# Kernel optimization log

Hardware: AMD Instinct MI355X
Metric: run time of the kernel (lower is better)

Reference implementation:

```python
import jax, jax.numpy as jnp
import numpy as np

GROUPS = 8


def setup_inputs() -> dict:
    key = jax.random.key(0)
    k1, k2, k3 = jax.random.split(key, 3)
    B, H, W, Cin, Cout, KH, KW = 32, 56, 56, 256, 256, 3, 3
    inputs = jax.random.normal(k1, (B, H, W, Cin), dtype=jnp.float32)
    # HWIO kernel for grouped conv: input channel dim = Cin // groups
    fan_in = KH * KW * (Cin // GROUPS)
    limit = np.sqrt(6.0 / (fan_in + Cout // GROUPS))  # glorot-ish scale
    kernel = jax.random.uniform(k2, (KH, KW, Cin // GROUPS, Cout), dtype=jnp.float32,
                                minval=-limit, maxval=limit)
    bias = jnp.zeros((Cout,), dtype=jnp.float32)
    return {"inputs": inputs, "kernel": kernel, "bias": bias}


def reference(inputs, kernel, bias):
    # Equivalent to per-group slice + Conv2D + concat: a single grouped conv.
    # inputs: [B,H,W,Cin] NHWC; kernel: [KH,KW,Cin//G,Cout] HWIO
    out = jax.lax.conv_general_dilated(
        inputs, kernel,
        window_strides=(1, 1),
        padding="SAME",
        lhs_dilation=(1, 1),
        rhs_dilation=(1, 1),
        dimension_numbers=("NHWC", "HWIO", "NHWC"),
        feature_group_count=GROUPS,
    )
    out = out + bias  # broadcast over [B,H,W,Cout]
    return out
```

## Files before the change

kernel.cpp:

```cpp
#include <hip/hip_runtime.h>


#define R_ 8
#define TPW 7

typedef __bf16 bf16x8 __attribute__((ext_vector_type(8)));
typedef float floatx4 __attribute__((ext_vector_type(4)));
typedef unsigned short ushortx4 __attribute__((ext_vector_type(4)));

__device__ __forceinline__ unsigned short f2bf(float f) {
    unsigned int u = __builtin_bit_cast(unsigned int, f);
    u += 0x7fffu + ((u >> 16) & 1u);
    return (unsigned short)(u >> 16);
}

__global__ __launch_bounds__(256)
void wprep(const float* __restrict__ wgt, unsigned short* __restrict__ wbf) {
    const int i = blockIdx.x * 256 + threadIdx.x;
    const int co256 = i & 255;
    const int tmp   = i >> 8;
    const int ci    = tmp & 31;
    const int kk    = tmp >> 5;
    const int g  = co256 >> 5;
    const int co = co256 & 31;
    wbf[((g * 9 + kk) * 32 + co) * 32 + ci] = f2bf(wgt[i]);
}

__global__ __launch_bounds__(256, 4)
void gconv_mfma(const float* __restrict__ in, const unsigned short* __restrict__ wbf,
                const float* __restrict__ bias, float* __restrict__ out) {
    const int rt = blockIdx.x;
    const int g  = blockIdx.y;
    const int b  = blockIdx.z;
    const int y0 = rt * R_;

    __shared__ unsigned short lds_in[10 * 58 * 32];

    const int tid = threadIdx.x;

    float4 v[19];
#pragma unroll
    for (int i = 0; i < 19; ++i) {
        const int c   = tid + (i << 8);
        const int row = c / 464;
        const int rem = c - row * 464;
        const int gy  = y0 - 1 + row;
        const int gx  = (rem >> 3) - 1;
        const bool ok = (c < 4640) & ((unsigned)gy < 56u) & ((unsigned)gx < 56u);
        const int gidx = ok ? ((((b * 56 + gy) * 56 + gx) << 8) + (g << 5) + ((rem & 7) << 2))
                            : 0;
        v[i] = *reinterpret_cast<const float4*>(&in[gidx]);
    }
#pragma unroll
    for (int i = 0; i < 19; ++i) {
        const int c = tid + (i << 8);
        if (c < 4640) {
            const int row = c / 464;
            const int rem = c - row * 464;
            const int gy  = y0 - 1 + row;
            const int gx  = (rem >> 3) - 1;
            float4 w = v[i];
            if (!(((unsigned)gy < 56u) & ((unsigned)gx < 56u)))
                w = make_float4(0.f, 0.f, 0.f, 0.f);
            ushortx4 p;
            p.x = f2bf(w.x); p.y = f2bf(w.y); p.z = f2bf(w.z); p.w = f2bf(w.w);
            *reinterpret_cast<ushortx4*>(
                &lds_in[(row * 58 + (rem >> 3)) * 32 + ((rem & 7) << 2)]) = p;
        }
    }

    __syncthreads();

    const int wv   = tid >> 6;
    const int lane = tid & 63;
    const int lc   = lane & 15;
    const int quad = lane >> 4;

    int lane_base[TPW];
#pragma unroll
    for (int t = 0; t < TPW; ++t) {
        const int p  = (wv * TPW + t) * 16 + lc;
        const int yl = p / 56;
        const int xl = p - yl * 56;
        lane_base[t] = (yl * 58 + xl) * 32 + (quad << 3);
    }

    const unsigned short* wq = &wbf[(g * 9 * 32) * 32 + (quad << 3)];

    floatx4 acc[TPW][2];
#pragma unroll
    for (int t = 0; t < TPW; ++t) {
        acc[t][0] = (floatx4)(0.f);
        acc[t][1] = (floatx4)(0.f);
    }

    bf16x8 b0 = *reinterpret_cast<const bf16x8*>(&wq[(0 * 32 + lc) * 32]);
    bf16x8 b1 = *reinterpret_cast<const bf16x8*>(&wq[(0 * 32 + 16 + lc) * 32]);

#pragma unroll
    for (int kk = 0; kk < 9; ++kk) {
        const int ky = kk / 3, kx = kk % 3;
        const int koff = (ky * 58 + kx) * 32;
        bf16x8 nb0 = b0, nb1 = b1;
        if (kk < 8) {
            nb0 = *reinterpret_cast<const bf16x8*>(&wq[((kk + 1) * 32 + lc) * 32]);
            nb1 = *reinterpret_cast<const bf16x8*>(&wq[((kk + 1) * 32 + 16 + lc) * 32]);
        }
#pragma unroll
        for (int t = 0; t < TPW; ++t) {
            const bf16x8 a = *reinterpret_cast<const bf16x8*>(&lds_in[lane_base[t] + koff]);
            acc[t][0] = __builtin_amdgcn_mfma_f32_16x16x32_bf16(b0, a, acc[t][0], 0, 0, 0);
            acc[t][1] = __builtin_amdgcn_mfma_f32_16x16x32_bf16(b1, a, acc[t][1], 0, 0, 0);
        }
        b0 = nb0; b1 = nb1;
    }

    const float4 bv0 = *reinterpret_cast<const float4*>(&bias[(g << 5) + (quad << 2)]);
    const float4 bv1 = *reinterpret_cast<const float4*>(&bias[(g << 5) + 16 + (quad << 2)]);
    const int obase = (((b * 56 + y0) * 56) << 8) + (g << 5) + (quad << 2);
#pragma unroll
    for (int t = 0; t < TPW; ++t) {
        const int p = (wv * TPW + t) * 16 + lc;
        const int y = p / 56;
        const int x = p - y * 56;
        float* o = &out[obase + ((y * 56 + x) << 8)];
        float4 s0, s1;
        s0.x = acc[t][0][0] + bv0.x; s0.y = acc[t][0][1] + bv0.y;
        s0.z = acc[t][0][2] + bv0.z; s0.w = acc[t][0][3] + bv0.w;
        s1.x = acc[t][1][0] + bv1.x; s1.y = acc[t][1][1] + bv1.y;
        s1.z = acc[t][1][2] + bv1.z; s1.w = acc[t][1][3] + bv1.w;
        *reinterpret_cast<float4*>(o)      = s0;
        *reinterpret_cast<float4*>(o + 16) = s1;
    }
}

__global__ __launch_bounds__(256, 2)
void gconv_mfma_ldsw(const float* __restrict__ in, const float* __restrict__ wgt,
                     const float* __restrict__ bias, float* __restrict__ out) {
    const int rt = blockIdx.x, g = blockIdx.y, b = blockIdx.z;
    const int y0 = rt * R_;
    __shared__ unsigned short lds_in[10 * 58 * 32];
    __shared__ unsigned short lds_w[9 * 32 * 32];
    const int tid = threadIdx.x;
    for (int i = tid; i < 9 * 32 * 32; i += 256) {
        const int co = i & 31, ci = (i >> 5) & 31, kk = i >> 10;
        lds_w[(kk * 32 + co) * 32 + ci] = f2bf(wgt[(kk * 32 + ci) * 256 + g * 32 + co]);
    }
    for (int c = tid; c < 10 * 58 * 8; c += 256) {
        const int row = c / 464, rem = c - row * 464, col = rem >> 3, q = rem & 7;
        const int gy = y0 - 1 + row, gx = col - 1;
        float4 v = make_float4(0.f, 0.f, 0.f, 0.f);
        if ((unsigned)gy < 56u && (unsigned)gx < 56u)
            v = *reinterpret_cast<const float4*>(&in[(((b * 56 + gy) * 56 + gx) * 256) + g * 32 + q * 4]);
        ushortx4 p;
        p.x = f2bf(v.x); p.y = f2bf(v.y); p.z = f2bf(v.z); p.w = f2bf(v.w);
        *reinterpret_cast<ushortx4*>(&lds_in[(row * 58 + col) * 32 + q * 4]) = p;
    }
    __syncthreads();
    const int wv = tid >> 6, lane = tid & 63, lc = lane & 15, quad = lane >> 4;
    int lane_base[TPW];
#pragma unroll
    for (int t = 0; t < TPW; ++t) {
        const int p = (wv * TPW + t) * 16 + lc;
        const int yl = p / 56, xl = p - yl * 56;
        lane_base[t] = (yl * 58 + xl) * 32 + quad * 8;
    }
    floatx4 acc[TPW][2];
#pragma unroll
    for (int t = 0; t < TPW; ++t) { acc[t][0] = (floatx4)(0.f); acc[t][1] = (floatx4)(0.f); }
#pragma unroll
    for (int kk = 0; kk < 9; ++kk) {
        const int ky = kk / 3, kx = kk % 3;
        const int koff = (ky * 58 + kx) * 32;
        const bf16x8 bf0 = *reinterpret_cast<const bf16x8*>(&lds_w[(kk * 32 + lc) * 32 + quad * 8]);
        const bf16x8 bf1 = *reinterpret_cast<const bf16x8*>(&lds_w[(kk * 32 + 16 + lc) * 32 + quad * 8]);
#pragma unroll
        for (int t = 0; t < TPW; ++t) {
            const bf16x8 a = *reinterpret_cast<const bf16x8*>(&lds_in[lane_base[t] + koff]);
            acc[t][0] = __builtin_amdgcn_mfma_f32_16x16x32_bf16(a, bf0, acc[t][0], 0, 0, 0);
            acc[t][1] = __builtin_amdgcn_mfma_f32_16x16x32_bf16(a, bf1, acc[t][1], 0, 0, 0);
        }
    }
    const float bv0 = bias[g * 32 + lc], bv1 = bias[g * 32 + 16 + lc];
#pragma unroll
    for (int t = 0; t < TPW; ++t)
#pragma unroll
        for (int r = 0; r < 4; ++r) {
            const int p = (wv * TPW + t) * 16 + quad * 4 + r;
            const int y = p / 56, x = p - y * 56;
            float* o = &out[(((b * 56) + y0 + y) * 56 + x) * 256 + g * 32];
            o[lc] = acc[t][0][r] + bv0;
            o[16 + lc] = acc[t][1][r] + bv1;
        }
}

extern "C" void kernel_launch(void* const* d_in, const int* in_sizes, int n_in,
                              void* d_out, int out_size, void* d_ws, size_t ws_size,
                              hipStream_t stream) {
    const float* in   = (const float*)d_in[0];
    const float* wgt  = (const float*)d_in[1];
    const float* bias = (const float*)d_in[2];
    float* out        = (float*)d_out;
    dim3 grid(7, 8, 32);

    if (ws_size >= (size_t)(8 * 9 * 32 * 32 * sizeof(unsigned short))) {
        unsigned short* wbf = (unsigned short*)d_ws;
        wprep<<<dim3(288, 1, 1), dim3(256, 1, 1), 0, stream>>>(wgt, wbf);
        gconv_mfma<<<grid, dim3(256, 1, 1), 0, stream>>>(in, wbf, bias, out);
    } else {
        gconv_mfma_ldsw<<<grid, dim3(256, 1, 1), 0, stream>>>(in, wgt, bias, out);
    }
}
```

Measured before the change: 197.7 us.

## Make conv blocks persistent over row tiles with double-buffered LDS prefetch

Replaces the one-tile-per-block grouped conv with a kernel of 512 blocks. Each block handles one (batch, group) pair and walks 3 or 4 row tiles, alternating by parity. While the MFMAs run on the current tile, it loads the next tile's input from global memory into registers, then writes it into a second LDS buffer. Weights for all 9 taps are held in registers once per block, which removes the repeated weight loads. In exchange, LDS use doubles, occupancy drops to 2 blocks per unit, and the 3-versus-4 tile split leaves the work unevenly balanced.

```diff
diff --git a/kernel.cpp b/kernel.cpp
--- a/kernel.cpp
+++ b/kernel.cpp
@@ -3,6 +3,7 @@
 
 #define R_ 8
 #define TPW 7
+#define NLOAD 19
 
 typedef __bf16 bf16x8 __attribute__((ext_vector_type(8)));
 typedef float floatx4 __attribute__((ext_vector_type(4)));
@@ -26,111 +27,126 @@
     wbf[((g * 9 + kk) * 32 + co) * 32 + ci] = f2bf(wgt[i]);
 }
 
-__global__ __launch_bounds__(256, 4)
-void gconv_mfma(const float* __restrict__ in, const unsigned short* __restrict__ wbf,
+__global__ __launch_bounds__(256, 2)
+void gconv_pipe(const float* __restrict__ in, const unsigned short* __restrict__ wbf,
                 const float* __restrict__ bias, float* __restrict__ out) {
-    const int rt = blockIdx.x;
-    const int g  = blockIdx.y;
-    const int b  = blockIdx.z;
-    const int y0 = rt * R_;
-
-    __shared__ unsigned short lds_in[10 * 58 * 32];
-
-    const int tid = threadIdx.x;
-
-    float4 v[19];
-#pragma unroll
-    for (int i = 0; i < 19; ++i) {
-        const int c   = tid + (i << 8);
-        const int row = c / 464;
-        const int rem = c - row * 464;
-        const int gy  = y0 - 1 + row;
-        const int gx  = (rem >> 3) - 1;
-        const bool ok = (c < 4640) & ((unsigned)gy < 56u) & ((unsigned)gx < 56u);
-        const int gidx = ok ? ((((b * 56 + gy) * 56 + gx) << 8) + (g << 5) + ((rem & 7) << 2))
-                            : 0;
-        v[i] = *reinterpret_cast<const float4*>(&in[gidx]);
-    }
-#pragma unroll
-    for (int i = 0; i < 19; ++i) {
-        const int c = tid + (i << 8);
-        if (c < 4640) {
+    const int h  = blockIdx.x & 1;
+    const int gb = blockIdx.x >> 1;
+    const int g  = gb & 7;
+    const int b  = gb >> 3;
+    const int ntiles = 4 - h;
+
+    __shared__ unsigned short lds_in[2][10 * 58 * 32];
+
+    const int tid  = threadIdx.x;
+    const int lane = tid & 63;
+    const int wv   = tid >> 6;
+    const int lc   = lane & 15;
+    const int quad = lane >> 4;
+
+    const unsigned short* wq = &wbf[(g * 9 * 32) * 32 + (quad << 3)];
+    bf16x8 w0[9], w1[9];
+#pragma unroll
+    for (int kk = 0; kk < 9; ++kk) {
+        w0[kk] = *reinterpret_cast<const bf16x8*>(&wq[(kk * 32 + lc) * 32]);
+        w1[kk] = *reinterpret_cast<const bf16x8*>(&wq[(kk * 32 + 16 + lc) * 32]);
+    }
+    const float4 bv0 = *reinterpret_cast<const float4*>(&bias[(g << 5) + (quad << 2)]);
+    const float4 bv1 = *reinterpret_cast<const float4*>(&bias[(g << 5) + 16 + (quad << 2)]);
+
+    int lane_base[TPW];
+#pragma unroll
+    for (int t = 0; t < TPW; ++t) {
+        const int p  = (wv * TPW + t) * 16 + lc;
+        const int yl = p / 56;
+        lane_base[t] = (yl * 58 + (p - yl * 56)) * 32 + (quad << 3);
+    }
+
+    const float* inb = &in[((b * 56 * 56) << 8)];
+
+    auto issue = [&](float4 (&v)[NLOAD], int y0) {
+#pragma unroll
+        for (int i = 0; i < NLOAD; ++i) {
+            const int c   = tid + (i << 8);
             const int row = c / 464;
             const int rem = c - row * 464;
             const int gy  = y0 - 1 + row;
             const int gx  = (rem >> 3) - 1;
-            float4 w = v[i];
-            if (!(((unsigned)gy < 56u) & ((unsigned)gx < 56u)))
-                w = make_float4(0.f, 0.f, 0.f, 0.f);
-            ushortx4 p;
-            p.x = f2bf(w.x); p.y = f2bf(w.y); p.z = f2bf(w.z); p.w = f2bf(w.w);
-            *reinterpret_cast<ushortx4*>(
-                &lds_in[(row * 58 + (rem >> 3)) * 32 + ((rem & 7) << 2)]) = p;
-        }
-    }
-
+            const bool ok = (c < 4640) & ((unsigned)gy < 56u) & ((unsigned)gx < 56u);
+            const int gidx = ok ? (((gy * 56 + gx) << 8) + (g << 5) + ((rem & 7) << 2)) : 0;
+            v[i] = *reinterpret_cast<const float4*>(&inb[gidx]);
+        }
+    };
+    auto commit = [&](const float4 (&v)[NLOAD], int y0, int buf) {
+#pragma unroll
+        for (int i = 0; i < NLOAD; ++i) {
+            const int c = tid + (i << 8);
+            if (c < 4640) {
+                const int row = c / 464;
+                const int rem = c - row * 464;
+                const int gy  = y0 - 1 + row;
+                const int gx  = (rem >> 3) - 1;
+                float4 w = v[i];
+                if (!(((unsigned)gy < 56u) & ((unsigned)gx < 56u)))
+                    w = make_float4(0.f, 0.f, 0.f, 0.f);
+                ushortx4 p;
+                p.x = f2bf(w.x); p.y = f2bf(w.y); p.z = f2bf(w.z); p.w = f2bf(w.w);
+                *reinterpret_cast<ushortx4*>(
+                    &lds_in[buf][(row * 58 + (rem >> 3)) * 32 + ((rem & 7) << 2)]) = p;
+            }
+        }
+    };
+
+    float4 v[NLOAD];
+
+    issue(v, h * R_);
+    commit(v, h * R_, 0);
     __syncthreads();
 
-    const int wv   = tid >> 6;
-    const int lane = tid & 63;
-    const int lc   = lane & 15;
-    const int quad = lane >> 4;
-
-    int lane_base[TPW];
-#pragma unroll
-    for (int t = 0; t < TPW; ++t) {
-        const int p  = (wv * TPW + t) * 16 + lc;
-        const int yl = p / 56;
-        const int xl = p - yl * 56;
-        lane_base[t] = (yl * 58 + xl) * 32 + (quad << 3);
-    }
-
-    const unsigned short* wq = &wbf[(g * 9 * 32) * 32 + (quad << 3)];
-
     floatx4 acc[TPW][2];
-#pragma unroll
-    for (int t = 0; t < TPW; ++t) {
-        acc[t][0] = (floatx4)(0.f);
-        acc[t][1] = (floatx4)(0.f);
-    }
-
-    bf16x8 b0 = *reinterpret_cast<const bf16x8*>(&wq[(0 * 32 + lc) * 32]);
-    bf16x8 b1 = *reinterpret_cast<const bf16x8*>(&wq[(0 * 32 + 16 + lc) * 32]);
-
-#pragma unroll
-    for (int kk = 0; kk < 9; ++kk) {
-        const int ky = kk / 3, kx = kk % 3;
-        const int koff = (ky * 58 + kx) * 32;
-        bf16x8 nb0 = b0, nb1 = b1;
-        if (kk < 8) {
-            nb0 = *reinterpret_cast<const bf16x8*>(&wq[((kk + 1) * 32 + lc) * 32]);
-            nb1 = *reinterpret_cast<const bf16x8*>(&wq[((kk + 1) * 32 + 16 + lc) * 32]);
-        }
+    int cur = 0;
+    for (int it = 0; it < ntiles; ++it) {
+        const int y0   = (h + 2 * it) * R_;
+        const bool more = (it + 1 < ntiles);
+
+        if (more) {
+            issue(v, y0 + 2 * R_);
+            __builtin_amdgcn_sched_barrier(0);
+        }
+
+#pragma unroll
+        for (int t = 0; t < TPW; ++t) { acc[t][0] = (floatx4)(0.f); acc[t][1] = (floatx4)(0.f); }
+#pragma unroll
+        for (int kk = 0; kk < 9; ++kk) {
+            const int koff = ((kk / 3) * 58 + (kk % 3)) * 32;
+#pragma unroll
+            for (int t = 0; t < TPW; ++t) {
+                const bf16x8 a = *reinterpret_cast<const bf16x8*>(
+                    &lds_in[cur][lane_base[t] + koff]);
+                acc[t][0] = __builtin_amdgcn_mfma_f32_16x16x32_bf16(w0[kk], a, acc[t][0], 0, 0, 0);
+                acc[t][1] = __builtin_amdgcn_mfma_f32_16x16x32_bf16(w1[kk], a, acc[t][1], 0, 0, 0);
+            }
+        }
+
+        if (more) commit(v, y0 + 2 * R_, cur ^ 1);
+        __syncthreads();
+
+        const int obase = (((b * 56 + y0) * 56) << 8) + (g << 5) + (quad << 2);
 #pragma unroll
         for (int t = 0; t < TPW; ++t) {
-            const bf16x8 a = *reinterpret_cast<const bf16x8*>(&lds_in[lane_base[t] + koff]);
-            acc[t][0] = __builtin_amdgcn_mfma_f32_16x16x32_bf16(b0, a, acc[t][0], 0, 0, 0);
-            acc[t][1] = __builtin_amdgcn_mfma_f32_16x16x32_bf16(b1, a, acc[t][1], 0, 0, 0);
-        }
-        b0 = nb0; b1 = nb1;
-    }
-
-    const float4 bv0 = *reinterpret_cast<const float4*>(&bias[(g << 5) + (quad << 2)]);
-    const float4 bv1 = *reinterpret_cast<const float4*>(&bias[(g << 5) + 16 + (quad << 2)]);
-    const int obase = (((b * 56 + y0) * 56) << 8) + (g << 5) + (quad << 2);
-#pragma unroll
-    for (int t = 0; t < TPW; ++t) {
-        const int p = (wv * TPW + t) * 16 + lc;
-        const int y = p / 56;
-        const int x = p - y * 56;
-        float* o = &out[obase + ((y * 56 + x) << 8)];
-        float4 s0, s1;
-        s0.x = acc[t][0][0] + bv0.x; s0.y = acc[t][0][1] + bv0.y;
-        s0.z = acc[t][0][2] + bv0.z; s0.w = acc[t][0][3] + bv0.w;
-        s1.x = acc[t][1][0] + bv1.x; s1.y = acc[t][1][1] + bv1.y;
-        s1.z = acc[t][1][2] + bv1.z; s1.w = acc[t][1][3] + bv1.w;
-        *reinterpret_cast<float4*>(o)      = s0;
-        *reinterpret_cast<float4*>(o + 16) = s1;
+            const int p = (wv * TPW + t) * 16 + lc;
+            const int y = p / 56;
+            const int x = p - y * 56;
+            float* o = &out[obase + ((y * 56 + x) << 8)];
+            float4 s0, s1;
+            s0.x = acc[t][0][0] + bv0.x; s0.y = acc[t][0][1] + bv0.y;
+            s0.z = acc[t][0][2] + bv0.z; s0.w = acc[t][0][3] + bv0.w;
+            s1.x = acc[t][1][0] + bv1.x; s1.y = acc[t][1][1] + bv1.y;
+            s1.z = acc[t][1][2] + bv1.z; s1.w = acc[t][1][3] + bv1.w;
+            *reinterpret_cast<float4*>(o)      = s0;
+            *reinterpret_cast<float4*>(o + 16) = s1;
+        }
+        cur ^= 1;
     }
 }
 
@@ -201,13 +217,12 @@
     const float* wgt  = (const float*)d_in[1];
     const float* bias = (const float*)d_in[2];
     float* out        = (float*)d_out;
-    dim3 grid(7, 8, 32);
 
     if (ws_size >= (size_t)(8 * 9 * 32 * 32 * sizeof(unsigned short))) {
         unsigned short* wbf = (unsigned short*)d_ws;
         wprep<<<dim3(288, 1, 1), dim3(256, 1, 1), 0, stream>>>(wgt, wbf);
-        gconv_mfma<<<grid, dim3(256, 1, 1), 0, stream>>>(in, wbf, bias, out);
+        gconv_pipe<<<dim3(512, 1, 1), dim3(256, 1, 1), 0, stream>>>(in, wbf, bias, out);
     } else {
-        gconv_mfma_ldsw<<<grid, dim3(256, 1, 1), 0, stream>>>(in, wgt, bias, out);
-    }
-}
+        gconv_mfma_ldsw<<<dim3(7, 8, 32), dim3(256, 1, 1), 0, stream>>>(in, wgt, bias, out);
+    }
+}
```

Result: slower. 252.8 us (+27.8%).
